# Kernel tuning notes

Hardware: AMD Instinct MI355X
Metric: run time of the kernel (lower is better)

The kernel has to match this reference:

```python
import jax, jax.numpy as jnp
import numpy as np

DIM = 512
NUM_HEADS = 8
HEAD_DIM = DIM // NUM_HEADS
EPS = 1e-05
BETA_INIT, TEMP_INIT, SHARP_INIT = 1.0, 0.5, 4.0


def setup_inputs() -> dict:
    key = jax.random.key(0)
    ks = jax.random.split(key, 9)
    b, t = 2, 1024
    s = 1.0 / np.sqrt(DIM)
    inp = {
        "x": jax.random.normal(ks[0], (b, t, DIM), dtype=jnp.float32),
        "wq_k": jax.random.normal(ks[1], (DIM, DIM), dtype=jnp.float32) * s,
        "wq_b": jnp.zeros((DIM,), dtype=jnp.float32),
        "wk_k": jax.random.normal(ks[2], (DIM, DIM), dtype=jnp.float32) * s,
        "wk_b": jnp.zeros((DIM,), dtype=jnp.float32),
        "wv_k": jax.random.normal(ks[3], (DIM, DIM), dtype=jnp.float32) * s,
        "wv_b": jnp.zeros((DIM,), dtype=jnp.float32),
        "wo_k": jax.random.normal(ks[4], (DIM, DIM), dtype=jnp.float32) * s,
        "wo_b": jnp.zeros((DIM,), dtype=jnp.float32),
        "log_beta": jnp.full((NUM_HEADS,), np.log(BETA_INIT), dtype=jnp.float32),
        "log_temp": jnp.full((NUM_HEADS,), np.log(TEMP_INIT), dtype=jnp.float32),
        "log_sharp": jnp.full((NUM_HEADS,), np.log(SHARP_INIT), dtype=jnp.float32),
    }
    return inp


def _softplus(x, beta):
    return (1.0 / beta) * jnp.log(1.0 + jnp.exp(beta * x))


def _combine(a, b):
    # log-domain combine: elements m (b,h,t,n), log_N (b,h,t,p,n), log_D (b,h,t,n)
    m_x, ln_x, ld_x = a
    m_y, ln_y, ld_y = b
    m_new = jnp.maximum(m_x, m_y)
    dx = m_x - m_new
    dy = m_y - m_new
    # note: (..., None) broadcast onto (b,h,t,p,n) works because p == n == HEAD_DIM
    ln_new = jnp.logaddexp(ln_x + dx[..., None], ln_y + dy[..., None])
    ld_new = jnp.logaddexp(ld_x + dx, ld_y + dy)
    return (m_new, ln_new, ld_new)


def reference(x, wq_k, wq_b, wk_k, wk_b, wv_k, wv_b, wo_k, wo_b,
              log_beta, log_temp, log_sharp):
    b, t, _ = x.shape
    q = (x @ wq_k + wq_b).reshape(b, t, NUM_HEADS, HEAD_DIM).transpose(0, 2, 1, 3)
    k = (x @ wk_k + wk_b).reshape(b, t, NUM_HEADS, HEAD_DIM).transpose(0, 2, 1, 3)
    v = (x @ wv_k + wv_b).reshape(b, t, NUM_HEADS, HEAD_DIM).transpose(0, 2, 1, 3)

    beta = jnp.exp(log_beta)[:, None, None]   # (h,1,1)
    temp = jnp.exp(log_temp)[:, None, None]
    sharp = jnp.exp(log_sharp)[:, None, None]

    q = q / temp
    k = k / temp
    Qf = _softplus(q, beta)  # (b,h,t,n)
    Kf = _softplus(k, beta)

    m0 = jnp.log(Kf + EPS)                         # (b,h,t,n)
    N0 = jnp.einsum('bhtp,bhtn->bhtpn', v, Kf)     # (b,h,t,p,n)
    D0 = Kf                                        # (b,h,t,n)

    m_c, N_c, D_c = jax.lax.associative_scan(_combine, (m0, N0, D0), axis=2)

    Y_num = jnp.einsum('bhtp,bhtpq->bhtq', Qf, N_c)
    Y_den = jnp.einsum('bhtp,bhtp->bht', Qf, D_c)
    Y = Y_num / (Y_den[..., None] + EPS)           # (b,h,t,n)
    Y = jnp.sign(Y) * jnp.abs(Y) ** sharp

    pos = (jnp.arange(1, t + 1, dtype=Y.dtype) / t).reshape(1, 1, t, 1)
    Y = Y * pos

    Y = Y.transpose(0, 2, 1, 3).reshape(b, t, DIM)
    return Y @ wo_k + wo_b
```

## Files before the change

kernel.cpp:

```cpp
#include <hip/hip_runtime.h>
#include <hip/hip_bf16.h>
#include <math.h>

#define DIM 512
#define NH 8
#define HD 64
#define TT 1024
#define CH 64
#define CL 16
#define EPSF 1e-5f
#define LN2F 0.69314718056f
#define LOG2EF 1.44269504089f

typedef unsigned short ushort_t;
typedef __attribute__((ext_vector_type(8))) short bf16x8;
typedef __attribute__((ext_vector_type(4))) float f32x4;

__device__ __forceinline__ float fexp2(float x) { return __builtin_amdgcn_exp2f(x); }
__device__ __forceinline__ float flog2(float x) { return __builtin_amdgcn_logf(x); }

__device__ __forceinline__ ushort_t f2bf(float f) {
    union { float f; unsigned u; } v; v.f = f;
    unsigned r = v.u + 0x7FFFu + ((v.u >> 16) & 1u);
    return (ushort_t)(r >> 16);
}
__device__ __forceinline__ float bf2f(ushort_t h) {
    union { unsigned u; float f; } v; v.u = ((unsigned)h) << 16;
    return v.f;
}

#define NXB 1024
__launch_bounds__(256)
__global__ void k_cvt(const float* __restrict__ x, ushort_t* __restrict__ xh,
                      ushort_t* __restrict__ xl,
                      const float* __restrict__ wq, const float* __restrict__ wk,
                      const float* __restrict__ wv, const float* __restrict__ wo,
                      ushort_t* __restrict__ wTh, ushort_t* __restrict__ wTl,
                      ushort_t* __restrict__ wTo)
{
    if (blockIdx.x < NXB) {
        int i = (blockIdx.x * 256 + threadIdx.x) * 4;
        float4 v = *(const float4*)&x[i];
        ushort4 h, l;
        h.x = f2bf(v.x); l.x = f2bf(v.x - bf2f(h.x));
        h.y = f2bf(v.y); l.y = f2bf(v.y - bf2f(h.y));
        h.z = f2bf(v.z); l.z = f2bf(v.z - bf2f(h.z));
        h.w = f2bf(v.w); l.w = f2bf(v.w - bf2f(h.w));
        *(ushort4*)&xh[i] = h;
        *(ushort4*)&xl[i] = l;
        return;
    }
    const int bid = blockIdx.x - NXB;
    const int mat = bid >> 5;
    const int rest = bid & 31;
    const int ky = rest >> 3, nx = rest & 7;
    const float* w = (mat == 0) ? wq : (mat == 1) ? wk : (mat == 2) ? wv : wo;
    const int n  = nx * 64 + (threadIdx.x & 63);
    const int k0 = ky * 128 + (threadIdx.x >> 6) * 32;

    ushort_t hb[32], lb[32];
#pragma unroll
    for (int j = 0; j < 32; j++) {
        float v = w[(size_t)(k0 + j) * DIM + n];
        hb[j] = f2bf(v);
        lb[j] = f2bf(v - bf2f(hb[j]));
    }
    if (mat < 3) {
        ushort_t* dh = wTh + (size_t)mat * DIM * DIM + (size_t)n * DIM + k0;
        ushort_t* dl = wTl + (size_t)mat * DIM * DIM + (size_t)n * DIM + k0;
#pragma unroll
        for (int j = 0; j < 8; j++) {
            ushort4 th = { hb[4*j], hb[4*j+1], hb[4*j+2], hb[4*j+3] };
            ushort4 tl = { lb[4*j], lb[4*j+1], lb[4*j+2], lb[4*j+3] };
            *(ushort4*)&dh[4*j] = th;
            *(ushort4*)&dl[4*j] = tl;
        }
    } else {
        ushort_t* dh = wTo + (size_t)n * DIM + k0;
#pragma unroll
        for (int j = 0; j < 8; j++) {
            ushort4 th = { hb[4*j], hb[4*j+1], hb[4*j+2], hb[4*j+3] };
            *(ushort4*)&dh[4*j] = th;
        }
    }
}

__launch_bounds__(256, 4)
__global__ void k_gemm_qkv(const ushort_t* __restrict__ xh, const ushort_t* __restrict__ xl,
                           const ushort_t* __restrict__ wTh, const ushort_t* __restrict__ wTl,
                           const float* __restrict__ bq, const float* __restrict__ bk,
                           const float* __restrict__ bv,
                           const float* __restrict__ lbeta, const float* __restrict__ ltemp,
                           float* __restrict__ Qf2, float* __restrict__ Kf,
                           float* __restrict__ Vv2)
{
    const int z = blockIdx.z, h = blockIdx.x;
    const int rowBase = blockIdx.y * 64;
    const int colBase = h * 64;
    const float* bias = (z == 0) ? bq : (z == 1) ? bk : bv;

    __shared__ __align__(16) ushort_t lds[2][4][2048];

    const int tid = threadIdx.x;
    const int l = tid & 63, wv = tid >> 6;
    const int m = l & 15, g = l >> 4;

    const int rl = tid >> 2, cc = tid & 3;
    const int ci = ((rl >> 4) * 64 + cc * 16 + (rl & 15)) * 8;
    const ushort_t* gAh = xh + (size_t)(rowBase + rl) * DIM + cc * 8;
    const ushort_t* gAl = xl + (size_t)(rowBase + rl) * DIM + cc * 8;
    const ushort_t* gBh = wTh + (size_t)z * DIM * DIM + (size_t)(colBase + rl) * DIM + cc * 8;
    const ushort_t* gBl = wTl + (size_t)z * DIM * DIM + (size_t)(colBase + rl) * DIM + cc * 8;

    f32x4 acc[4] = { {0,0,0,0}, {0,0,0,0}, {0,0,0,0}, {0,0,0,0} };

    {
        bf16x8 a0 = *(const bf16x8*)gAh;
        bf16x8 a1 = *(const bf16x8*)gAl;
        bf16x8 b0 = *(const bf16x8*)gBh;
        bf16x8 b1 = *(const bf16x8*)gBl;
        *(bf16x8*)&lds[0][0][ci] = a0;
        *(bf16x8*)&lds[0][1][ci] = a1;
        *(bf16x8*)&lds[0][2][ci] = b0;
        *(bf16x8*)&lds[0][3][ci] = b1;
    }
    __syncthreads();

    for (int it = 0; it < 16; ++it) {
        const int cur = it & 1;
        bf16x8 nAh, nAl, nBh, nBl;
        if (it < 15) {
            const int K = (it + 1) * 32;
            nAh = *(const bf16x8*)(gAh + K);
            nAl = *(const bf16x8*)(gAl + K);
            nBh = *(const bf16x8*)(gBh + K);
            nBl = *(const bf16x8*)(gBl + K);
        }
        bf16x8 ah = *(const bf16x8*)&lds[cur][0][tid * 8];
        bf16x8 al = *(const bf16x8*)&lds[cur][1][tid * 8];
#pragma unroll
        for (int n = 0; n < 4; n++) {
            bf16x8 bh = *(const bf16x8*)&lds[cur][2][(n * 64 + l) * 8];
            bf16x8 bl = *(const bf16x8*)&lds[cur][3][(n * 64 + l) * 8];
            acc[n] = __builtin_amdgcn_mfma_f32_16x16x32_bf16(ah, bh, acc[n], 0, 0, 0);
            acc[n] = __builtin_amdgcn_mfma_f32_16x16x32_bf16(al, bh, acc[n], 0, 0, 0);
            acc[n] = __builtin_amdgcn_mfma_f32_16x16x32_bf16(ah, bl, acc[n], 0, 0, 0);
        }
        if (it < 15) {
            const int nxt = cur ^ 1;
            *(bf16x8*)&lds[nxt][0][ci] = nAh;
            *(bf16x8*)&lds[nxt][1][ci] = nAl;
            *(bf16x8*)&lds[nxt][2][ci] = nBh;
            *(bf16x8*)&lds[nxt][3][ci] = nBl;
            __syncthreads();
        }
    }

    if (z == 2) {
#pragma unroll
        for (int n = 0; n < 4; n++) {
            int c = n * 16 + m;
            float bval = bias[colBase + c];
#pragma unroll
            for (int r = 0; r < 4; r++) {
                int rr = rowBase + wv * 16 + g * 4 + r;
                int bb = rr >> 10, t = rr & (TT - 1);
                Vv2[(((size_t)(bb * NH + h)) * TT + t) * HD + c] = (acc[n][r] + bval) * LOG2EF;
            }
        }
    } else {
        float beta = expf(lbeta[h]);
        float itemp = 1.0f / expf(ltemp[h]);
        float oscale = (z == 0) ? (LN2F / beta) : (1.0f / beta);
        float* __restrict__ dst = (z == 0) ? Qf2 : Kf;
#pragma unroll
        for (int n = 0; n < 4; n++) {
            int c = n * 16 + m;
            float bval = bias[colBase + c];
#pragma unroll
            for (int r = 0; r < 4; r++) {
                int rr = rowBase + wv * 16 + g * 4 + r;
                int bb = rr >> 10, t = rr & (TT - 1);
                float val = (acc[n][r] + bval) * itemp;
                float zz = beta * val;
                float sp = (fmaxf(zz, 0.f) + log1pf(expf(-fabsf(zz)))) * oscale;
                dst[(((size_t)(bb * NH + h)) * TT + t) * HD + c] = sp;
            }
        }
    }
}

__launch_bounds__(256)
__global__ void k_chunk_reduce(const float* __restrict__ Kf, const float* __restrict__ Vv2,
                               float* __restrict__ aA, float* __restrict__ aD,
                               float* __restrict__ aCM)
{
    const int c = blockIdx.x >> 1, qh = blockIdx.x & 1;
    const int bh = blockIdx.z * NH + blockIdx.y;
    const int tid = threadIdx.x;

    __shared__ __align__(16) float sK[CL * HD];
    __shared__ __align__(16) float sV2[CL * HD];
    __shared__ __align__(16) float sM02[CL * HD];

    size_t base = ((size_t)bh * TT + (size_t)c * CL) * HD;
    const float4* K4 = (const float4*)(Kf + base);
    const float4* V4 = (const float4*)(Vv2 + base);
    {
        int f = tid;
        float4 kv = K4[f];
        ((float4*)sK)[f] = kv;
        float4 mm;
        mm.x = flog2(kv.x + EPSF); mm.y = flog2(kv.y + EPSF);
        mm.z = flog2(kv.z + EPSF); mm.w = flog2(kv.w + EPSF);
        ((float4*)sM02)[f] = mm;
        ((float4*)sV2)[f] = V4[f];
    }
    __syncthreads();

    const int p = tid & 63, qo = tid >> 6;
    const int q0 = qh * 32 + qo * 8;
    float A[8] = {};
    float AD = 0.f, cmx = 0.f;
    const bool doD = (qh == 0) && (tid < 64);

#pragma unroll
    for (int s = 0; s < CL; s++) {
        float vp = sV2[s * HD + p];
        float mp = sM02[s * HD + p];
        float4 ka = *(const float4*)&sK[s * HD + q0];
        float4 kb = *(const float4*)&sK[s * HD + q0 + 4];
        A[0] += fexp2(fmaf(vp, ka.x, mp));
        A[1] += fexp2(fmaf(vp, ka.y, mp));
        A[2] += fexp2(fmaf(vp, ka.z, mp));
        A[3] += fexp2(fmaf(vp, ka.w, mp));
        A[4] += fexp2(fmaf(vp, kb.x, mp));
        A[5] += fexp2(fmaf(vp, kb.y, mp));
        A[6] += fexp2(fmaf(vp, kb.z, mp));
        A[7] += fexp2(fmaf(vp, kb.w, mp));
        if (doD) {
            float kn = sK[s * HD + tid];
            float ke = kn + EPSF;
            AD += fexp2(kn * LOG2EF) * ke;
            cmx = fmaxf(cmx, ke);
        }
    }

    size_t abase = ((size_t)bh * CH + c) * 4096 + (size_t)p * HD + q0;
    float4 o0 = { A[0], A[1], A[2], A[3] };
    float4 o1 = { A[4], A[5], A[6], A[7] };
    *(float4*)&aA[abase] = o0;
    *(float4*)&aA[abase + 4] = o1;
    if (doD) {
        size_t dbase = ((size_t)bh * CH + c) * HD + tid;
        aD[dbase] = AD; aCM[dbase] = cmx;
    }
}

__global__ void k_scan_agg(float* __restrict__ aA, float* __restrict__ aD,
                           float* __restrict__ aCM, int BH)
{
    int idx = blockIdx.x * 256 + threadIdx.x;
    int nA4 = BH * 1024;
    int nD4 = BH * 16;
    if (idx < nA4) {
        int bh = idx >> 10, pn4 = (idx & 1023) * 4;
        float4 Sr = {0.f, 0.f, 0.f, 0.f};
        for (int c = 0; c < CH; c++) {
            float* p = &aA[((size_t)bh * CH + c) * 4096 + pn4];
            float4 t = *(float4*)p;
            *(float4*)p = Sr;
            Sr.x += t.x; Sr.y += t.y; Sr.z += t.z; Sr.w += t.w;
        }
    } else if (idx < nA4 + nD4) {
        int i = idx - nA4; int bh = i >> 4, n4 = (i & 15) * 4;
        float4 Sr = {0.f, 0.f, 0.f, 0.f};
        for (int c = 0; c < CH; c++) {
            float* p = &aD[((size_t)bh * CH + c) * HD + n4];
            float4 t = *(float4*)p;
            *(float4*)p = Sr;
            Sr.x += t.x; Sr.y += t.y; Sr.z += t.z; Sr.w += t.w;
        }
    } else if (idx < nA4 + 2 * nD4) {
        int i = idx - nA4 - nD4; int bh = i >> 4, n4 = (i & 15) * 4;
        float4 r = {0.f, 0.f, 0.f, 0.f};
        for (int c = 0; c < CH; c++) {
            float* p = &aCM[((size_t)bh * CH + c) * HD + n4];
            float4 t = *(float4*)p;
            *(float4*)p = r;
            r.x = fmaxf(r.x, t.x); r.y = fmaxf(r.y, t.y);
            r.z = fmaxf(r.z, t.z); r.w = fmaxf(r.w, t.w);
        }
    }
}

__launch_bounds__(64)
__global__ void k_den(const float* __restrict__ Kf, const float* __restrict__ Qf2,
                      const float* __restrict__ aD, const float* __restrict__ aCM,
                      float* __restrict__ c1f, float* __restrict__ invd)
{
    const int c = blockIdx.x;
    const int bh = blockIdx.z * NH + blockIdx.y;
    const int n = threadIdx.x;
    size_t dbase = ((size_t)bh * CH + c) * HD + n;
    float AD = aD[dbase], cmx = aCM[dbase];
    size_t base = ((size_t)bh * TT + (size_t)c * CL) * HD + n;
    float* outc = c1f + (size_t)bh * TT + c * CL;
    float* outi = invd + (size_t)bh * TT + c * CL;

    for (int s = 0; s < CL; s++) {
        float kn = Kf[base + (size_t)s * HD];
        float qn = Qf2[base + (size_t)s * HD];
        float ke = kn + EPSF;
        AD += fexp2(kn * LOG2EF) * ke;
        cmx = fmaxf(cmx, ke);
        float t1 = qn * flog2(cmx);
        float t2 = qn * flog2(AD);
#pragma unroll
        for (int off = 1; off <= 32; off <<= 1) {
            t1 += __shfl_xor(t1, off);
            t2 += __shfl_xor(t2, off);
        }
        if (n == 0) {
            outc[s] = t1;
            outi[s] = 1.0f / (t2 - t1 + EPSF);
        }
    }
}

__launch_bounds__(256)
__global__ void k_chunk_out(const float* __restrict__ Kf, const float* __restrict__ Vv2,
                            const float* __restrict__ Qf2, const float* __restrict__ aA,
                            const float* __restrict__ c1f, const float* __restrict__ invd,
                            const float* __restrict__ lsharp, ushort_t* __restrict__ Ymb)
{
    const int c = blockIdx.x, hh = blockIdx.y, bb = blockIdx.z;
    const int bh = bb * NH + hh;
    const int tid = threadIdx.x;

    __shared__ __align__(16) float sK[CL * HD];
    __shared__ __align__(16) float sV2[CL * HD];
    __shared__ __align__(16) float sM02[CL * HD];
    __shared__ __align__(16) float sQ2[CL * HD];

    size_t base = ((size_t)bh * TT + (size_t)c * CL) * HD;
    const float4* K4 = (const float4*)(Kf + base);
    const float4* V4 = (const float4*)(Vv2 + base);
    const float4* Q4 = (const float4*)(Qf2 + base);
    {
        int f = tid;
        float4 kv = K4[f];
        ((float4*)sK)[f] = kv;
        float4 mm;
        mm.x = flog2(kv.x + EPSF); mm.y = flog2(kv.y + EPSF);
        mm.z = flog2(kv.z + EPSF); mm.w = flog2(kv.w + EPSF);
        ((float4*)sM02)[f] = mm;
        ((float4*)sV2)[f] = V4[f];
        ((float4*)sQ2)[f] = Q4[f];
    }
    __syncthreads();

    const int lane = tid & 63, w = tid >> 6;
    const int g = lane >> 3, qil = lane & 7;
    const int qA = w * 8 + qil, qB = qA + 32;
    const int p0 = g * 8;

    float A[8], Bq[8];
    size_t abase = ((size_t)bh * CH + c) * 4096;
#pragma unroll
    for (int j = 0; j < 8; j++) {
        A[j]  = aA[abase + (size_t)(p0 + j) * HD + qA];
        Bq[j] = aA[abase + (size_t)(p0 + j) * HD + qB];
    }
    const float sharp = expf(lsharp[hh]);
    const float invT = 1.0f / (float)TT;
    const float* c1p = c1f + (size_t)bh * TT + c * CL;
    const float* ivp = invd + (size_t)bh * TT + c * CL;

#pragma unroll 4
    for (int s = 0; s < CL; s++) {
        float kqA = sK[s * HD + qA];
        float kqB = sK[s * HD + qB];
        float pA0 = 0.f, pA1 = 0.f, pB0 = 0.f, pB1 = 0.f;
#pragma unroll
        for (int j4 = 0; j4 < 2; j4++) {
            float4 vv = *(const float4*)&sV2[s * HD + p0 + j4 * 4];
            float4 mm = *(const float4*)&sM02[s * HD + p0 + j4 * 4];
            float4 qv = *(const float4*)&sQ2[s * HD + p0 + j4 * 4];
#define STEP(comp, jj, PA, PB) { \
            A[jj]  += fexp2(fmaf(vv.comp, kqA, mm.comp)); \
            PA = fmaf(qv.comp, flog2(A[jj]), PA); \
            Bq[jj] += fexp2(fmaf(vv.comp, kqB, mm.comp)); \
            PB = fmaf(qv.comp, flog2(Bq[jj]), PB); }
            STEP(x, j4 * 4 + 0, pA0, pB0)
            STEP(y, j4 * 4 + 1, pA1, pB1)
            STEP(z, j4 * 4 + 2, pA0, pB0)
            STEP(w, j4 * 4 + 3, pA1, pB1)
#undef STEP
        }
        float partA = pA0 + pA1;
        float partB = pB0 + pB1;
        partA += __shfl_xor(partA, 8);
        partA += __shfl_xor(partA, 16);
        partA += __shfl_xor(partA, 32);
        partB += __shfl_xor(partB, 8);
        partB += __shfl_xor(partB, 16);
        partB += __shfl_xor(partB, 32);

        float c1v = c1p[s], iv = ivp[s];
        int tg = c * CL + s;
        float scale = (float)(tg + 1) * invT;
        float yA = (partA - c1v) * iv;
        float yB = (partB - c1v) * iv;
        float oA = copysignf(fexp2(sharp * flog2(fabsf(yA))), yA) * scale;
        float oB = copysignf(fexp2(sharp * flog2(fabsf(yB))), yB) * scale;
        if (g == 0) {
            ushort_t* yrow = Ymb + ((size_t)(bb * TT + tg)) * DIM + hh * HD;
            yrow[qA] = f2bf(oA);
            yrow[qB] = f2bf(oB);
        }
    }
}

__launch_bounds__(256, 4)
__global__ void k_gemm_out(const ushort_t* __restrict__ Ymb, const ushort_t* __restrict__ wTo,
                           const float* __restrict__ bias, float* __restrict__ out)
{
    const int colBase = blockIdx.x * 64;
    const int rowBase = blockIdx.y * 32;

    __shared__ __align__(16) ushort_t sA[2][1024];
    __shared__ __align__(16) ushort_t sB[2][2048];

    const int tid = threadIdx.x;
    const int l = tid & 63, wv = tid >> 6;
    const int m = l & 15, g = l >> 4;
    const int wr = wv & 1, wc = wv >> 1;

    const int rlB = tid >> 2, ccB = tid & 3;
    const int ciB = ((rlB >> 4) * 64 + ccB * 16 + (rlB & 15)) * 8;
    const ushort_t* gB = wTo + (size_t)(colBase + rlB) * DIM + ccB * 8;
    const int rlA = (tid & 127) >> 2, ccA = tid & 3;
    const int ciA = ((rlA >> 4) * 64 + ccA * 16 + (rlA & 15)) * 8;
    const ushort_t* gA = Ymb + (size_t)(rowBase + rlA) * DIM + ccA * 8;
    const bool doA = tid < 128;

    f32x4 acc[2] = { {0,0,0,0}, {0,0,0,0} };

    {
        bf16x8 b0 = *(const bf16x8*)gB;
        *(bf16x8*)&sB[0][ciB] = b0;
        if (doA) {
            bf16x8 a0 = *(const bf16x8*)gA;
            *(bf16x8*)&sA[0][ciA] = a0;
        }
    }
    __syncthreads();

    for (int it = 0; it < 16; ++it) {
        const int cur = it & 1;
        bf16x8 nA, nB;
        if (it < 15) {
            const int K = (it + 1) * 32;
            nB = *(const bf16x8*)(gB + K);
            if (doA) nA = *(const bf16x8*)(gA + K);
        }
        bf16x8 a = *(const bf16x8*)&sA[cur][(wr * 64 + l) * 8];
#pragma unroll
        for (int n = 0; n < 2; n++) {
            bf16x8 b = *(const bf16x8*)&sB[cur][((wc * 2 + n) * 64 + l) * 8];
            acc[n] = __builtin_amdgcn_mfma_f32_16x16x32_bf16(a, b, acc[n], 0, 0, 0);
        }
        if (it < 15) {
            const int nxt = cur ^ 1;
            *(bf16x8*)&sB[nxt][ciB] = nB;
            if (doA) *(bf16x8*)&sA[nxt][ciA] = nA;
            __syncthreads();
        }
    }

#pragma unroll
    for (int n = 0; n < 2; n++) {
        int c = colBase + wc * 32 + n * 16 + m;
        float bval = bias[c];
#pragma unroll
        for (int r = 0; r < 4; r++) {
            int rr = rowBase + wr * 16 + g * 4 + r;
            out[(size_t)rr * DIM + c] = acc[n][r] + bval;
        }
    }
}

extern "C" void kernel_launch(void* const* d_in, const int* in_sizes, int n_in,
                              void* d_out, int out_size, void* d_ws, size_t ws_size,
                              hipStream_t stream)
{
    const float* x  = (const float*)d_in[0];
    const float* wq = (const float*)d_in[1];
    const float* bq = (const float*)d_in[2];
    const float* wk = (const float*)d_in[3];
    const float* bk = (const float*)d_in[4];
    const float* wv = (const float*)d_in[5];
    const float* bv = (const float*)d_in[6];
    const float* wo = (const float*)d_in[7];
    const float* bo = (const float*)d_in[8];
    const float* lb = (const float*)d_in[9];
    const float* lt = (const float*)d_in[10];
    const float* ls = (const float*)d_in[11];

    const int B  = in_sizes[0] / (TT * DIM);
    const int BH = B * NH;

    float* ws = (float*)d_ws;
    const size_t nQ = (size_t)BH * TT * HD;
    float* Qf2 = ws;
    float* Kf  = Qf2 + nQ;
    float* Vv2 = Kf + nQ;
    float* region = Vv2 + nQ;

    ushort_t* xh  = (ushort_t*)region;
    ushort_t* xl  = xh + (size_t)B * TT * DIM;
    ushort_t* wTh = (ushort_t*)(region + (size_t)B * TT * DIM);
    ushort_t* wTl = wTh + (size_t)3 * DIM * DIM;
    ushort_t* Ymb = (ushort_t*)region;
    float* aA  = region + (size_t)B * TT * DIM;
    float* aD  = aA  + (size_t)BH * CH * 4096;
    float* aCM = aD  + (size_t)BH * CH * HD;
    float* c1f = aCM + (size_t)BH * CH * HD;
    float* invd= c1f + (size_t)BH * TT;
    ushort_t* wTo = (ushort_t*)(invd + (size_t)BH * TT);

    k_cvt<<<NXB + 128, 256, 0, stream>>>(x, xh, xl, wq, wk, wv, wo, wTh, wTl, wTo);

    dim3 g1(NH, (B * TT) / 64, 3);
    k_gemm_qkv<<<g1, 256, 0, stream>>>(xh, xl, wTh, wTl, bq, bk, bv, lb, lt, Qf2, Kf, Vv2);

    dim3 g2(CH * 2, NH, B);
    k_chunk_reduce<<<g2, 256, 0, stream>>>(Kf, Vv2, aA, aD, aCM);

    int ntot = BH * 1024 + 2 * BH * 16;
    k_scan_agg<<<(ntot + 255) / 256, 256, 0, stream>>>(aA, aD, aCM, BH);

    dim3 g4(CH, NH, B);
    k_den<<<g4, 64, 0, stream>>>(Kf, Qf2, aD, aCM, c1f, invd);

    k_chunk_out<<<g4, 256, 0, stream>>>(Kf, Vv2, Qf2, aA, c1f, invd, ls, Ymb);

    dim3 g6(DIM / 64, (B * TT) / 32);
    k_gemm_out<<<g6, 256, 0, stream>>>(Ymb, wTo, bo, (float*)d_out);
}
```

Measured before the change: 95.44 us.

## Fuse denominator kernel into chunk output and use 2x2 warp tiling in QKV GEMM

```diff
diff --git a/kernel.cpp b/kernel.cpp
--- a/kernel.cpp
+++ b/kernel.cpp
@@ -104,6 +104,7 @@
     const int tid = threadIdx.x;
     const int l = tid & 63, wv = tid >> 6;
     const int m = l & 15, g = l >> 4;
+    const int wr = wv & 1, wc = wv >> 1;
 
     const int rl = tid >> 2, cc = tid & 3;
     const int ci = ((rl >> 4) * 64 + cc * 16 + (rl & 15)) * 8;
@@ -112,7 +113,7 @@
     const ushort_t* gBh = wTh + (size_t)z * DIM * DIM + (size_t)(colBase + rl) * DIM + cc * 8;
     const ushort_t* gBl = wTl + (size_t)z * DIM * DIM + (size_t)(colBase + rl) * DIM + cc * 8;
 
-    f32x4 acc[4] = { {0,0,0,0}, {0,0,0,0}, {0,0,0,0}, {0,0,0,0} };
+    f32x4 acc[2][2] = { { {0,0,0,0}, {0,0,0,0} }, { {0,0,0,0}, {0,0,0,0} } };
 
     {
         bf16x8 a0 = *(const bf16x8*)gAh;
@@ -136,16 +137,25 @@
             nBh = *(const bf16x8*)(gBh + K);
             nBl = *(const bf16x8*)(gBl + K);
         }
-        bf16x8 ah = *(const bf16x8*)&lds[cur][0][tid * 8];
-        bf16x8 al = *(const bf16x8*)&lds[cur][1][tid * 8];
-#pragma unroll
-        for (int n = 0; n < 4; n++) {
-            bf16x8 bh = *(const bf16x8*)&lds[cur][2][(n * 64 + l) * 8];
-            bf16x8 bl = *(const bf16x8*)&lds[cur][3][(n * 64 + l) * 8];
-            acc[n] = __builtin_amdgcn_mfma_f32_16x16x32_bf16(ah, bh, acc[n], 0, 0, 0);
-            acc[n] = __builtin_amdgcn_mfma_f32_16x16x32_bf16(al, bh, acc[n], 0, 0, 0);
-            acc[n] = __builtin_amdgcn_mfma_f32_16x16x32_bf16(ah, bl, acc[n], 0, 0, 0);
-        }
+        bf16x8 ah[2], al[2], bh[2], bl[2];
+#pragma unroll
+        for (int rf = 0; rf < 2; rf++) {
+            ah[rf] = *(const bf16x8*)&lds[cur][0][((wr * 2 + rf) * 64 + l) * 8];
+            al[rf] = *(const bf16x8*)&lds[cur][1][((wr * 2 + rf) * 64 + l) * 8];
+        }
+#pragma unroll
+        for (int cf = 0; cf < 2; cf++) {
+            bh[cf] = *(const bf16x8*)&lds[cur][2][((wc * 2 + cf) * 64 + l) * 8];
+            bl[cf] = *(const bf16x8*)&lds[cur][3][((wc * 2 + cf) * 64 + l) * 8];
+        }
+#pragma unroll
+        for (int rf = 0; rf < 2; rf++)
+#pragma unroll
+            for (int cf = 0; cf < 2; cf++) {
+                acc[rf][cf] = __builtin_amdgcn_mfma_f32_16x16x32_bf16(ah[rf], bh[cf], acc[rf][cf], 0, 0, 0);
+                acc[rf][cf] = __builtin_amdgcn_mfma_f32_16x16x32_bf16(al[rf], bh[cf], acc[rf][cf], 0, 0, 0);
+                acc[rf][cf] = __builtin_amdgcn_mfma_f32_16x16x32_bf16(ah[rf], bl[cf], acc[rf][cf], 0, 0, 0);
+            }
         if (it < 15) {
             const int nxt = cur ^ 1;
             *(bf16x8*)&lds[nxt][0][ci] = nAh;
@@ -158,35 +168,39 @@
 
     if (z == 2) {
 #pragma unroll
-        for (int n = 0; n < 4; n++) {
-            int c = n * 16 + m;
-            float bval = bias[colBase + c];
-#pragma unroll
-            for (int r = 0; r < 4; r++) {
-                int rr = rowBase + wv * 16 + g * 4 + r;
-                int bb = rr >> 10, t = rr & (TT - 1);
-                Vv2[(((size_t)(bb * NH + h)) * TT + t) * HD + c] = (acc[n][r] + bval) * LOG2EF;
+        for (int rf = 0; rf < 2; rf++)
+#pragma unroll
+            for (int cf = 0; cf < 2; cf++) {
+                int c = wc * 32 + cf * 16 + m;
+                float bval = bias[colBase + c];
+#pragma unroll
+                for (int r = 0; r < 4; r++) {
+                    int rr = rowBase + wr * 32 + rf * 16 + g * 4 + r;
+                    int bb = rr >> 10, t = rr & (TT - 1);
+                    Vv2[(((size_t)(bb * NH + h)) * TT + t) * HD + c] = (acc[rf][cf][r] + bval) * LOG2EF;
+                }
             }
-        }
     } else {
         float beta = expf(lbeta[h]);
         float itemp = 1.0f / expf(ltemp[h]);
         float oscale = (z == 0) ? (LN2F / beta) : (1.0f / beta);
         float* __restrict__ dst = (z == 0) ? Qf2 : Kf;
 #pragma unroll
-        for (int n = 0; n < 4; n++) {
-            int c = n * 16 + m;
-            float bval = bias[colBase + c];
-#pragma unroll
-            for (int r = 0; r < 4; r++) {
-                int rr = rowBase + wv * 16 + g * 4 + r;
-                int bb = rr >> 10, t = rr & (TT - 1);
-                float val = (acc[n][r] + bval) * itemp;
-                float zz = beta * val;
-                float sp = (fmaxf(zz, 0.f) + log1pf(expf(-fabsf(zz)))) * oscale;
-                dst[(((size_t)(bb * NH + h)) * TT + t) * HD + c] = sp;
+        for (int rf = 0; rf < 2; rf++)
+#pragma unroll
+            for (int cf = 0; cf < 2; cf++) {
+                int c = wc * 32 + cf * 16 + m;
+                float bval = bias[colBase + c];
+#pragma unroll
+                for (int r = 0; r < 4; r++) {
+                    int rr = rowBase + wr * 32 + rf * 16 + g * 4 + r;
+                    int bb = rr >> 10, t = rr & (TT - 1);
+                    float val = (acc[rf][cf][r] + bval) * itemp;
+                    float zz = beta * val;
+                    float sp = (fmaxf(zz, 0.f) + log1pf(expf(-fabsf(zz)))) * oscale;
+                    dst[(((size_t)(bb * NH + h)) * TT + t) * HD + c] = sp;
+                }
             }
-        }
     }
 }
 
@@ -294,44 +308,10 @@
     }
 }
 
-__launch_bounds__(64)
-__global__ void k_den(const float* __restrict__ Kf, const float* __restrict__ Qf2,
-                      const float* __restrict__ aD, const float* __restrict__ aCM,
-                      float* __restrict__ c1f, float* __restrict__ invd)
-{
-    const int c = blockIdx.x;
-    const int bh = blockIdx.z * NH + blockIdx.y;
-    const int n = threadIdx.x;
-    size_t dbase = ((size_t)bh * CH + c) * HD + n;
-    float AD = aD[dbase], cmx = aCM[dbase];
-    size_t base = ((size_t)bh * TT + (size_t)c * CL) * HD + n;
-    float* outc = c1f + (size_t)bh * TT + c * CL;
-    float* outi = invd + (size_t)bh * TT + c * CL;
-
-    for (int s = 0; s < CL; s++) {
-        float kn = Kf[base + (size_t)s * HD];
-        float qn = Qf2[base + (size_t)s * HD];
-        float ke = kn + EPSF;
-        AD += fexp2(kn * LOG2EF) * ke;
-        cmx = fmaxf(cmx, ke);
-        float t1 = qn * flog2(cmx);
-        float t2 = qn * flog2(AD);
-#pragma unroll
-        for (int off = 1; off <= 32; off <<= 1) {
-            t1 += __shfl_xor(t1, off);
-            t2 += __shfl_xor(t2, off);
-        }
-        if (n == 0) {
-            outc[s] = t1;
-            outi[s] = 1.0f / (t2 - t1 + EPSF);
-        }
-    }
-}
-
 __launch_bounds__(256)
 __global__ void k_chunk_out(const float* __restrict__ Kf, const float* __restrict__ Vv2,
                             const float* __restrict__ Qf2, const float* __restrict__ aA,
-                            const float* __restrict__ c1f, const float* __restrict__ invd,
+                            const float* __restrict__ aD, const float* __restrict__ aCM,
                             const float* __restrict__ lsharp, ushort_t* __restrict__ Ymb)
 {
     const int c = blockIdx.x, hh = blockIdx.y, bb = blockIdx.z;
@@ -342,6 +322,7 @@
     __shared__ __align__(16) float sV2[CL * HD];
     __shared__ __align__(16) float sM02[CL * HD];
     __shared__ __align__(16) float sQ2[CL * HD];
+    __shared__ float sC1[CL], sIV[CL];
 
     size_t base = ((size_t)bh * TT + (size_t)c * CL) * HD;
     const float4* K4 = (const float4*)(Kf + base);
@@ -372,10 +353,36 @@
         A[j]  = aA[abase + (size_t)(p0 + j) * HD + qA];
         Bq[j] = aA[abase + (size_t)(p0 + j) * HD + qB];
     }
+
+    {
+        size_t dofs = ((size_t)bh * CH + c) * HD + lane;
+        float AD = aD[dofs], cmx = aCM[dofs];
+#pragma unroll
+        for (int s = 0; s < CL; s++) {
+            float kn = sK[s * HD + lane];
+            float ke = kn + EPSF;
+            AD += fexp2(kn * LOG2EF) * ke;
+            cmx = fmaxf(cmx, ke);
+            if ((s & 3) == w) {
+                float qn = sQ2[s * HD + lane];
+                float t1 = qn * flog2(cmx);
+                float t2 = qn * flog2(AD);
+#pragma unroll
+                for (int off = 1; off <= 32; off <<= 1) {
+                    t1 += __shfl_xor(t1, off);
+                    t2 += __shfl_xor(t2, off);
+                }
+                if (lane == 0) {
+                    sC1[s] = t1;
+                    sIV[s] = 1.0f / (t2 - t1 + EPSF);
+                }
+            }
+        }
+    }
+    __syncthreads();
+
     const float sharp = expf(lsharp[hh]);
     const float invT = 1.0f / (float)TT;
-    const float* c1p = c1f + (size_t)bh * TT + c * CL;
-    const float* ivp = invd + (size_t)bh * TT + c * CL;
 
 #pragma unroll 4
     for (int s = 0; s < CL; s++) {
@@ -407,7 +414,7 @@
         partB += __shfl_xor(partB, 16);
         partB += __shfl_xor(partB, 32);
 
-        float c1v = c1p[s], iv = ivp[s];
+        float c1v = sC1[s], iv = sIV[s];
         int tg = c * CL + s;
         float scale = (float)(tg + 1) * invT;
         float yA = (partA - c1v) * iv;
@@ -526,9 +533,7 @@
     float* aA  = region + (size_t)B * TT * DIM;
     float* aD  = aA  + (size_t)BH * CH * 4096;
     float* aCM = aD  + (size_t)BH * CH * HD;
-    float* c1f = aCM + (size_t)BH * CH * HD;
-    float* invd= c1f + (size_t)BH * TT;
-    ushort_t* wTo = (ushort_t*)(invd + (size_t)BH * TT);
+    ushort_t* wTo = (ushort_t*)(aCM + (size_t)BH * CH * HD);
 
     k_cvt<<<NXB + 128, 256, 0, stream>>>(x, xh, xl, wq, wk, wv, wo, wTh, wTl, wTo);
 
@@ -542,9 +547,7 @@
     k_scan_agg<<<(ntot + 255) / 256, 256, 0, stream>>>(aA, aD, aCM, BH);
 
     dim3 g4(CH, NH, B);
-    k_den<<<g4, 64, 0, stream>>>(Kf, Qf2, aD, aCM, c1f, invd);
-
-    k_chunk_out<<<g4, 256, 0, stream>>>(Kf, Vv2, Qf2, aA, c1f, invd, ls, Ymb);
+    k_chunk_out<<<g4, 256, 0, stream>>>(Kf, Vv2, Qf2, aA, aD, aCM, ls, Ymb);
 
     dim3 g6(DIM / 64, (B * TT) / 32);
     k_gemm_out<<<g6, 256, 0, stream>>>(Ymb, wTo, bo, (float*)d_out);
```

Measured after the change: 89.05 us. 6.7% less time.
